# Optimization experiments

Measured on AMD Instinct MI355X. Metric: run time of the kernel, lower is better.

## Reference

```python
import jax, jax.numpy as jnp
import numpy as np
from functools import partial

A_CUBIC = -0.75  # PyTorch grid_sample bicubic coefficient

def _cubic_weights(t):
    # t in [0,1); returns 4 weights for taps at offsets -1,0,1,2
    a = A_CUBIC
    t2 = t * t; t3 = t2 * t
    w0 = a * (t3 - 2.0 * t2 + t)
    w1 = (a + 2.0) * t3 - (a + 3.0) * t2 + 1.0
    s = 1.0 - t
    w2 = (a + 2.0) * s * s * s - (a + 3.0) * s * s + 1.0
    u = 2.0 - t
    w3 = a * u * u * u - 5.0 * a * u * u + 8.0 * a * u - 4.0 * a
    return (w0, w1, w2, w3)

def grid_sample_bicubic(img, gx, gy):
    # img [N,C,H,W]; gx,gy [N,Ho,Wo] normalized coords in [-1,1]; border padding, align_corners=False
    N, C, H, W = img.shape
    ix = ((gx + 1.0) * W - 1.0) * 0.5
    iy = ((gy + 1.0) * H - 1.0) * 0.5
    x0 = jnp.floor(ix); tx = ix - x0
    y0 = jnp.floor(iy); ty = iy - y0
    x0i = x0.astype(jnp.int32); y0i = y0.astype(jnp.int32)
    wx = _cubic_weights(tx); wy = _cubic_weights(ty)
    gather = jax.vmap(lambda im, yi, xi: im[:, yi, xi])  # per-sample [C,Ho,Wo]
    out = jnp.zeros((N, C) + gx.shape[1:], img.dtype)
    for i in range(4):
        yi = jnp.clip(y0i + (i - 1), 0, H - 1)
        for j in range(4):
            xj = jnp.clip(x0i + (j - 1), 0, W - 1)
            v = gather(img, yi, xj)
            out = out + (wy[i] * wx[j])[:, None] * v
    return out

def jitter_aligned_interp(img, jitter, f):
    # F.affine_grid(identity+translation) + grid_sample bicubic, align_corners=False
    N, C, H, W = img.shape
    Ho, Wo = H * f, W * f
    bx = (2.0 * jnp.arange(Wo, dtype=img.dtype) + 1.0) / Wo - 1.0
    by = (2.0 * jnp.arange(Ho, dtype=img.dtype) + 1.0) / Ho - 1.0
    tx = 2.0 * (0.5 - jitter[:, 0]) / W
    ty = 2.0 * (0.5 - jitter[:, 1]) / H
    gx = jnp.broadcast_to(bx[None, None, :] + tx[:, None, None], (N, Ho, Wo))
    gy = jnp.broadcast_to(by[None, :, None] + ty[:, None, None], (N, Ho, Wo))
    return grid_sample_bicubic(img, gx, gy)

def zero_upsample(x, f):
    N, C, H, W = x.shape
    out = jnp.zeros((N, C, H * f, W * f), x.dtype)
    return out.at[:, :, ::f, ::f].set(x)

def jitter_align(img, jitter, f):
    # pad by f, per-sample crop at integer jitter offset (zero constant pad)
    N, C, H, W = img.shape
    ji = jnp.floor(jitter * f).astype(jnp.int32)  # [N,2] (x,y)
    padded = jnp.pad(img, ((0, 0), (0, 0), (f, f), (f, f)))
    def crop(im, j):
        sy = f - j[1]; sx = f - j[0]
        return jax.lax.dynamic_slice(im, (0, sy, sx), (C, H, W))
    return jax.vmap(crop)(padded, ji)

def resize_bilinear(x, f):
    # F.interpolate bilinear, align_corners=False (half-pixel, clamp to >=0 and edges)
    N, C, H, W = x.shape
    def coords(L):
        c = jnp.maximum((jnp.arange(L * f, dtype=x.dtype) + 0.5) / f - 0.5, 0.0)
        i0 = jnp.floor(c); t = c - i0
        i0 = i0.astype(jnp.int32)
        return jnp.clip(i0, 0, L - 1), jnp.clip(i0 + 1, 0, L - 1), t
    y0, y1, tyv = coords(H)
    x0, x1, txv = coords(W)
    xr = x[:, :, y0, :] * (1.0 - tyv)[None, None, :, None] + x[:, :, y1, :] * tyv[None, None, :, None]
    return xr[:, :, :, x0] * (1.0 - txv) + xr[:, :, :, x1] * txv

def conv3x3_reppad(x, w, b):
    x = jnp.pad(x, ((0, 0), (0, 0), (1, 1), (1, 1)), mode='edge')
    y = jax.lax.conv_general_dilated(x, w, (1, 1), 'VALID',
                                     dimension_numbers=('NCHW', 'OIHW', 'NCHW'))
    return y + b[None, :, None, None]

def sub_forward(frame, depth, mv, jitter, history, params, f):
    w1, b1, w2, b2, w3, b3 = params
    N = frame.shape[0]
    far, near = 100.0, 0.1
    d = near * far / (far - depth * (far - near))
    d = (d - near) / (far - near)
    frame4 = jnp.concatenate([frame, d], axis=1)  # [N,4,H,W]
    frame_bicubic = jitter_aligned_interp(frame4, jitter, f)  # [N,4,Hf,Wf]
    frame_up = jitter_align(zero_upsample(frame4, f), jitter, f)
    if history is None:
        history = frame_bicubic
    else:
        mv_hi = resize_bilinear(jnp.moveaxis(mv, 3, 1), f)       # [N,2,Hf,Wf]
        mv_hi = jnp.moveaxis(mv_hi, 1, 3)                        # [N,Hf,Wf,2]
        history = grid_sample_bicubic(history, mv_hi[..., 0], mv_hi[..., 1])
        oob = jnp.logical_or(mv_hi > 1.0, mv_hi < -1.0)
        mask = jnp.logical_or(oob[..., 0], oob[..., 1])[:, None]  # [N,1,Hf,Wf]
        history = jnp.where(mask, frame_bicubic, history)
    cnn_in = jnp.concatenate([frame_up, history], axis=1)  # [N,8,Hf,Wf]
    h = jax.nn.relu(conv3x3_reppad(cnn_in, w1, b1))
    h = jax.nn.relu(conv3x3_reppad(h, w2, b2))
    residual = conv3x3_reppad(h, w3, b3)  # [N,2,Hf,Wf]
    alpha = jnp.clip(residual[:, 0:1], 0.0, 1.0)
    history = history * (1.0 - alpha) + frame_bicubic * alpha
    history = jnp.concatenate([history[:, :3], history[:, 3:4] + residual[:, 1:2]], axis=1)
    history = jnp.clip(history, 0.0, 1.0)
    return history[:, :3], history

FACTOR = 2

def setup_inputs() -> dict:
    key = jax.random.key(0)
    ks = jax.random.split(key, 10)
    T, N, H, W = 3, 2, 360, 640
    frames = jax.random.uniform(ks[0], (T, N, 3, H, W), jnp.float32)
    depths = jax.random.uniform(ks[1], (T, N, 1, H, W), jnp.float32)
    mvs = jax.random.uniform(ks[2], (T, N, H, W, 2), jnp.float32, -1.05, 1.05)
    jitters = jax.random.uniform(ks[3], (T, N, 2), jnp.float32)
    w1 = jax.random.normal(ks[4], (64, 8, 3, 3), jnp.float32) * 0.1
    b1 = jnp.zeros((64,), jnp.float32)
    w2 = jax.random.normal(ks[5], (64, 64, 3, 3), jnp.float32) * 0.04
    b2 = jnp.zeros((64,), jnp.float32)
    w3 = jax.random.normal(ks[6], (2, 64, 3, 3), jnp.float32) * 0.04
    b3 = jnp.zeros((2,), jnp.float32)
    return {"frames": frames, "depths": depths, "mvs": mvs, "jitters": jitters,
            "w1": w1, "b1": b1, "w2": w2, "b2": b2, "w3": w3, "b3": b3}

def reference(frames, depths, mvs, jitters, w1, b1, w2, b2, w3, b3):
    params = (w1, b1, w2, b2, w3, b3)
    T = frames.shape[0]
    history = None
    outs = []
    for t in range(T - 1, -1, -1):  # torch forward iterates seq_length-1 .. 0
        recon, history = sub_forward(frames[t], depths[t], mvs[t], jitters[t], history, params, FACTOR)
        outs.append(recon)
    outs.reverse()
    return jnp.stack(outs)  # [T,N,3,H*f,W*f]
```

## Files before the change

kernel.cpp:

```cpp
#include <hip/hip_runtime.h>

#define T_STEPS 3
#define NB 2
#define H_LO 360
#define W_LO 640
#define H_HI 720
#define W_HI 1280
#define HW_LO (H_LO*W_LO)
#define HW_HI (H_HI*W_HI)
#define TILE 12

typedef _Float16 f16;
typedef __attribute__((ext_vector_type(4))) _Float16 f16x4;
typedef __attribute__((ext_vector_type(8))) _Float16 f16x8;
typedef __attribute__((ext_vector_type(4))) float f32x4;

#define OFF_H1  0
#define OFF_H2  0
#define OFF_CNN 32768
#define OFF_RES 32768
#define LDS_BYTES 37952

__device__ __forceinline__ int imin(int a,int b){return a<b?a:b;}
__device__ __forceinline__ int imax(int a,int b){return a>b?a:b;}
__device__ __forceinline__ int iclamp(int v,int lo,int hi){return imin(imax(v,lo),hi);}

__device__ __forceinline__ float depth_tx(float d0){
  float d = 10.0f / (100.0f - d0*99.9f);
  return (d - 0.1f) / 99.9f;
}

__device__ __forceinline__ void cubw(float t, float* w){
  const float a = -0.75f;
  float t2 = t*t, t3 = t2*t;
  w[0] = a*(t3 - 2.0f*t2 + t);
  w[1] = (a+2.0f)*t3 - (a+3.0f)*t2 + 1.0f;
  float s = 1.0f - t;
  w[2] = (a+2.0f)*s*s*s - (a+3.0f)*s*s + 1.0f;
  float u = 2.0f - t;
  w[3] = a*u*u*u - 5.0f*a*u*u + 8.0f*a*u - 4.0f*a;
}

__device__ __forceinline__ float4 fb_bicubic(const float* __restrict__ fbase,
    const float* __restrict__ dbase, float jx, float jy, int x, int y){
  float gx = (2.0f*(float)x + 1.0f)/(float)W_HI - 1.0f + 2.0f*(0.5f - jx)/(float)W_LO;
  float gy = (2.0f*(float)y + 1.0f)/(float)H_HI - 1.0f + 2.0f*(0.5f - jy)/(float)H_LO;
  float ix = ((gx + 1.0f)*(float)W_LO - 1.0f)*0.5f;
  float iy = ((gy + 1.0f)*(float)H_LO - 1.0f)*0.5f;
  float xf = floorf(ix), yf = floorf(iy);
  float tx = ix - xf, ty = iy - yf;
  int xi = (int)xf, yi = (int)yf;
  float wx[4], wy[4]; cubw(tx, wx); cubw(ty, wy);
  int xs[4], ys[4];
  #pragma unroll
  for (int j=0;j<4;j++){ xs[j]=iclamp(xi-1+j,0,W_LO-1); ys[j]=iclamp(yi-1+j,0,H_LO-1); }
  float a0=0.f,a1=0.f,a2=0.f,a3=0.f;
  #pragma unroll
  for (int i=0;i<4;i++){
    #pragma unroll
    for (int j=0;j<4;j++){
      float wgt = wy[i]*wx[j];
      int off = ys[i]*W_LO + xs[j];
      a0 += wgt*fbase[off];
      a1 += wgt*fbase[HW_LO+off];
      a2 += wgt*fbase[2*HW_LO+off];
      a3 += wgt*depth_tx(dbase[off]);
    }
  }
  return make_float4(a0,a1,a2,a3);
}

__global__ __launch_bounds__(256) void k_wprep(const float* __restrict__ w1g,
    const float* __restrict__ w2g, const float* __restrict__ w3g, f16* __restrict__ wbuf){
  int i = blockIdx.x*256 + threadIdx.x;
  if (i >= 46592) return;
  float val = 0.0f;
  if (i < 8192){
    int oc = i>>7, kk = i&127, k = kk ^ ((oc&7)<<3);
    if (k < 72) val = w1g[(oc*8 + (k&7))*9 + (k>>3)];
  } else if (i < 45056){
    int j = i - 8192; int oc = j/576, kk = j - oc*576, k = kk ^ ((oc&7)<<3);
    val = w2g[(oc*64 + (k&63))*9 + (k>>6)];
  } else {
    int j = i - 45056;
    if (j < 1152){ int nn = j/576, k = j - nn*576;
      val = w3g[(nn*64 + (k&63))*9 + (k>>6)];
    }
  }
  wbuf[i] = (f16)val;
}

__global__ __launch_bounds__(256) void k_pw(const float4* __restrict__ histA,
    const float* __restrict__ mv, const float* __restrict__ frame,
    const float* __restrict__ depth, const float* __restrict__ jit,
    float4* __restrict__ FB, float4* __restrict__ histB, int doWarp){
  int idx = blockIdx.x*256 + threadIdx.x;
  if (idx >= NB*HW_HI) return;
  int n = idx / HW_HI, p = idx - n*HW_HI;
  int y = p / W_HI, x = p - y*W_HI;
  const float* fbase = frame + (size_t)n*3*HW_LO;
  const float* dbase = depth + (size_t)n*HW_LO;
  float4 fb4 = fb_bicubic(fbase, dbase, jit[n*2], jit[n*2+1], x, y);
  FB[(size_t)n*HW_HI + p] = fb4;
  if (!doWarp) return;

  float cy = fmaxf(((float)y + 0.5f)/2.0f - 0.5f, 0.0f);
  float cx = fmaxf(((float)x + 0.5f)/2.0f - 0.5f, 0.0f);
  float y0f = floorf(cy), x0f = floorf(cx);
  float tyv = cy - y0f, txv = cx - x0f;
  int y0 = iclamp((int)y0f, 0, H_LO-1), y1 = iclamp((int)y0f+1, 0, H_LO-1);
  int x0 = iclamp((int)x0f, 0, W_LO-1), x1 = iclamp((int)x0f+1, 0, W_LO-1);
  const float* mb = mv + (size_t)n*HW_LO*2;
  float gx, gy;
  {
    float v00 = mb[(y0*W_LO+x0)*2], v01 = mb[(y0*W_LO+x1)*2];
    float v10 = mb[(y1*W_LO+x0)*2], v11 = mb[(y1*W_LO+x1)*2];
    float r0 = v00*(1.0f-tyv) + v10*tyv;
    float r1 = v01*(1.0f-tyv) + v11*tyv;
    gx = r0*(1.0f-txv) + r1*txv;
  }
  {
    float v00 = mb[(y0*W_LO+x0)*2+1], v01 = mb[(y0*W_LO+x1)*2+1];
    float v10 = mb[(y1*W_LO+x0)*2+1], v11 = mb[(y1*W_LO+x1)*2+1];
    float r0 = v00*(1.0f-tyv) + v10*tyv;
    float r1 = v01*(1.0f-tyv) + v11*tyv;
    gy = r0*(1.0f-txv) + r1*txv;
  }
  bool oob = (gx > 1.0f) || (gx < -1.0f) || (gy > 1.0f) || (gy < -1.0f);
  float4 res;
  if (oob) {
    res = fb4;
  } else {
    const float4* hb = histA + (size_t)n*HW_HI;
    float ix = ((gx + 1.0f)*(float)W_HI - 1.0f)*0.5f;
    float iy = ((gy + 1.0f)*(float)H_HI - 1.0f)*0.5f;
    float xf = floorf(ix), yf = floorf(iy);
    float tx = ix - xf, ty = iy - yf;
    int xi = (int)xf, yi = (int)yf;
    float wx[4], wy[4]; cubw(tx, wx); cubw(ty, wy);
    int xs[4], ys[4];
    #pragma unroll
    for (int j=0;j<4;j++){ xs[j]=iclamp(xi-1+j,0,W_HI-1); ys[j]=iclamp(yi-1+j,0,H_HI-1); }
    float a0=0.f,a1=0.f,a2=0.f,a3=0.f;
    #pragma unroll
    for (int i=0;i<4;i++){
      #pragma unroll
      for (int j=0;j<4;j++){
        float wgt = wy[i]*wx[j];
        float4 v = hb[ys[i]*W_HI + xs[j]];
        a0 += wgt*v.x; a1 += wgt*v.y; a2 += wgt*v.z; a3 += wgt*v.w;
      }
    }
    res = make_float4(a0,a1,a2,a3);
  }
  histB[(size_t)n*HW_HI + p] = res;
}

__global__ __launch_bounds__(256,3) void k_fused(
    const float* __restrict__ frame, const float* __restrict__ depth,
    const float* __restrict__ jit, const float4* __restrict__ histIn,
    const float4* __restrict__ FB, const f16* __restrict__ wbuf,
    const float* __restrict__ b1g, const float* __restrict__ b2g, const float* __restrict__ b3g,
    float4* __restrict__ histOut, float* __restrict__ outp)
{
  __shared__ __attribute__((aligned(16))) char smem[LDS_BYTES];
  const int tid = threadIdx.x;
  const int wv = tid>>6, ln = tid&63, lr = ln&15, lq = ln>>4;
  const int n  = blockIdx.z;
  const int r0 = blockIdx.y * TILE;
  const int c0 = blockIdx.x * TILE;
  const float jx = jit[n*2], jy = jit[n*2+1];
  const int jix = (int)floorf(jx*2.0f), jiy = (int)floorf(jy*2.0f);
  const float* fbase = frame + (size_t)n*3*HW_LO;
  const float* dbase = depth + (size_t)n*HW_LO;
  const float4* hist4 = histIn + (size_t)n*HW_HI;
  const int wkk = (lr&7)<<3;

  f16x8 B1[3][4];
  #pragma unroll
  for (int kc=0;kc<3;kc++)
    #pragma unroll
    for (int oct=0;oct<4;oct++){
      int oc = oct*16 + lr;
      int k0 = kc*32 + lq*8;
      B1[kc][oct] = *(const f16x8*)(wbuf + oc*128 + (k0 ^ wkk));
    }

  for (int e=tid; e<324; e+=256){
    int u = e/18, v = e - u*18;
    int cgy = iclamp(r0-3+u, 0, H_HI-1);
    int cgx = iclamp(c0-3+v, 0, W_HI-1);
    float v0=0.f, v1=0.f, v2=0.f, v3=0.f;
    int yy = cgy - jiy, xx = cgx - jix;
    if (yy>=0 && xx>=0 && !(yy&1) && !(xx&1)){
      int off = (yy>>1)*W_LO + (xx>>1);
      v0 = fbase[off]; v1 = fbase[HW_LO+off]; v2 = fbase[2*HW_LO+off];
      v3 = depth_tx(dbase[off]);
    }
    float4 h = hist4[cgy*W_HI + cgx];
    f16x8 pk;
    pk[0]=(f16)v0; pk[1]=(f16)v1; pk[2]=(f16)v2; pk[3]=(f16)v3;
    pk[4]=(f16)h.x; pk[5]=(f16)h.y; pk[6]=(f16)h.z; pk[7]=(f16)h.w;
    *(f16x8*)(smem + OFF_CNN + e*16) = pk;
  }
  __syncthreads();

  {
    float4 b1v[4];
    #pragma unroll
    for (int oct=0;oct<4;oct++) b1v[oct] = *(const float4*)(b1g + oct*16 + lq*4);
    #pragma unroll
    for (int ty4=0;ty4<4;ty4++){
      int ty = wv*4 + ty4;
      int g1y = iclamp(r0-2+ty, 0, H_HI-1);
      int g1x = iclamp(c0-2+lr, 0, W_HI-1);
      f32x4 acc[4];
      #pragma unroll
      for (int oct=0;oct<4;oct++) acc[oct] = (f32x4){b1v[oct].x,b1v[oct].y,b1v[oct].z,b1v[oct].w};
      #pragma unroll
      for (int kc=0;kc<3;kc++){
        int k0 = kc*32 + lq*8;
        int t = imin(k0>>3, 8);
        int dy = (t*11)>>5; int dx = t - dy*3;
        int uu = iclamp(g1y+dy-1, 0, H_HI-1) - (r0-3);
        int vv = iclamp(g1x+dx-1, 0, W_HI-1) - (c0-3);
        f16x8 a = *(const f16x8*)(smem + OFF_CNN + (uu*18+vv)*16);
        #pragma unroll
        for (int oct=0;oct<4;oct++)
          acc[oct] = __builtin_amdgcn_mfma_f32_16x16x32_f16(B1[kc][oct], a, acc[oct], 0,0,0);
      }
      #pragma unroll
      for (int oct=0;oct<4;oct++){
        f16x4 wv4;
        #pragma unroll
        for (int reg=0;reg<4;reg++) wv4[reg] = (f16)fmaxf(acc[oct][reg], 0.f);
        int oc0 = (oct*16 + lq*4) ^ ((lr&7)<<3);
        *(f16x4*)(smem + OFF_H1 + (((ty*16+lr)*64 + oc0)<<1)) = wv4;
      }
    }
  }
  __syncthreads();

  {
    const int nmt = (wv==0) ? 4 : 3;
    const int mtid[4] = {wv, 4+wv, 8+wv, 12};
    int rowOf[4][3], colc[4][3][2];
    #pragma unroll
    for (int mti=0;mti<4;mti++){
      int m = imin(mtid[mti]*16 + lr, 195);
      int py = m/14, px = m - py*14;
      int Ay = iclamp(r0-1+py, 0, H_HI-1);
      int Ax = iclamp(c0-1+px, 0, W_HI-1);
      #pragma unroll
      for (int d=0;d<3;d++){
        rowOf[mti][d] = (iclamp(Ay+d-1, 0, H_HI-1) - (r0-2))*1024;
        int vv = iclamp(Ax+d-1, 0, W_HI-1) - (c0-2);
        int key = (vv&7)<<3;
        colc[mti][d][0] = vv*64 + ((lq*8) ^ key);
        colc[mti][d][1] = vv*64 + ((32+lq*8) ^ key);
      }
    }
    float4 b2v[4];
    #pragma unroll
    for (int oct=0;oct<4;oct++) b2v[oct] = *(const float4*)(b2g + oct*16 + lq*4);
    f32x4 acc2[4][4];
    #pragma unroll
    for (int mti=0;mti<4;mti++)
      #pragma unroll
      for (int oct=0;oct<4;oct++) acc2[mti][oct] = (f32x4){b2v[oct].x,b2v[oct].y,b2v[oct].z,b2v[oct].w};
    const f16* w2b = wbuf + 8192;
    f16x8 bf[4];
    #pragma unroll
    for (int oct=0;oct<4;oct++)
      bf[oct] = *(const f16x8*)(w2b + (oct*16+lr)*576 + ((lq*8) ^ wkk));
    #pragma unroll
    for (int kc=0;kc<18;kc++){
      const int tap = kc>>1, half = kc&1;
      const int dy = tap/3, dx = tap - dy*3;
      f16x8 bfn[4];
      if (kc < 17){
        const int kn = kc+1, tapn = kn>>1, halfn = kn&1;
        #pragma unroll
        for (int oct=0;oct<4;oct++)
          bfn[oct] = *(const f16x8*)(w2b + (oct*16+lr)*576 + ((tapn*64 + halfn*32 + lq*8) ^ wkk));
      }
      #pragma unroll
      for (int mti=0;mti<4;mti++) if (mti < nmt){
        f16x8 a = *(const f16x8*)(smem + OFF_H1 + ((rowOf[mti][dy] + colc[mti][dx][half])<<1));
        #pragma unroll
        for (int oct=0;oct<4;oct++)
          acc2[mti][oct] = __builtin_amdgcn_mfma_f32_16x16x32_f16(bf[oct], a, acc2[mti][oct], 0,0,0);
      }
      #pragma unroll
      for (int oct=0;oct<4;oct++) bf[oct] = bfn[oct];
    }
    __syncthreads();
    #pragma unroll
    for (int mti=0;mti<4;mti++) if (mti < nmt){
      int m = mtid[mti]*16 + lr;
      if (m < 196){
        int py = m/14, px = m - py*14;
        int base = (py*14+px)*64; int key = (px&7)<<3;
        #pragma unroll
        for (int oct=0;oct<4;oct++){
          f16x4 wv4;
          #pragma unroll
          for (int reg=0;reg<4;reg++) wv4[reg] = (f16)fmaxf(acc2[mti][oct][reg], 0.f);
          *(f16x4*)(smem + OFF_H2 + ((base + ((oct*16 + lq*4) ^ key))<<1)) = wv4;
        }
      }
    }
  }
  __syncthreads();

  {
    const int nm3 = (wv==0) ? 3 : 2;
    const int m3t[3] = {wv, 4+wv, 8};
    int rowOf[3][3], colc[3][3][2];
    #pragma unroll
    for (int i=0;i<3;i++){
      int m = m3t[i]*16 + lr;
      int py = m/12, px = m - py*12;
      int Cy = r0 + py;
      int Cx = iclamp(c0+px, 0, W_HI-1);
      #pragma unroll
      for (int d=0;d<3;d++){
        rowOf[i][d] = (iclamp(Cy+d-1, 0, H_HI-1) - (r0-1))*896;
        int vv = iclamp(Cx+d-1, 0, W_HI-1) - (c0-1);
        int key = (vv&7)<<3;
        colc[i][d][0] = vv*64 + ((lq*8) ^ key);
        colc[i][d][1] = vv*64 + ((32+lq*8) ^ key);
      }
    }
    f32x4 acc3[3] = {{0,0,0,0},{0,0,0,0},{0,0,0,0}};
    const int cidx = ln&1;
    const f16* w3b = wbuf + 45056;
    f16x8 b = *(const f16x8*)(w3b + cidx*576 + lq*8);
    #pragma unroll
    for (int kc=0;kc<18;kc++){
      const int tap = kc>>1, half = kc&1;
      const int dy = tap/3, dx = tap - dy*3;
      f16x8 bn;
      if (kc < 17) bn = *(const f16x8*)(w3b + cidx*576 + (kc+1)*32 + lq*8);
      #pragma unroll
      for (int i=0;i<3;i++) if (i < nm3){
        f16x8 a = *(const f16x8*)(smem + OFF_H2 + ((rowOf[i][dy] + colc[i][dx][half])<<1));
        acc3[i] = __builtin_amdgcn_mfma_f32_16x16x32_f16(a, b, acc3[i], 0,0,0);
      }
      b = bn;
    }
    __syncthreads();
    float* sres = (float*)(smem + OFF_RES);
    if (lr < 2){
      float bv = b3g[lr];
      #pragma unroll
      for (int i=0;i<3;i++) if (i < nm3){
        #pragma unroll
        for (int reg=0;reg<4;reg++){
          int m = m3t[i]*16 + lq*4 + reg;
          sres[lr*144 + m] = acc3[i][reg] + bv;
        }
      }
    }
  }
  __syncthreads();

  if (tid < 144){
    int ty = tid/12, tx = tid - ty*12;
    int gy = r0 + ty, gx = c0 + tx;
    if (gx < W_HI){
      const float* sres = (const float*)(smem + OFF_RES);
      float a0 = sres[tid], a1 = sres[144+tid];
      float alpha = fminf(fmaxf(a0, 0.0f), 1.0f);
      int pix = gy*W_HI + gx;
      float4 fb = FB[(size_t)n*HW_HI + pix];
      float4 hv = hist4[pix];
      float h0 = hv.x*(1.0f-alpha) + fb.x*alpha;
      float h1 = hv.y*(1.0f-alpha) + fb.y*alpha;
      float h2 = hv.z*(1.0f-alpha) + fb.z*alpha;
      float h3 = hv.w*(1.0f-alpha) + fb.w*alpha + a1;
      h0 = fminf(fmaxf(h0,0.f),1.f); h1 = fminf(fmaxf(h1,0.f),1.f);
      h2 = fminf(fmaxf(h2,0.f),1.f); h3 = fminf(fmaxf(h3,0.f),1.f);
      histOut[(size_t)n*HW_HI + pix] = make_float4(h0,h1,h2,h3);
      float* rp = outp + (size_t)n*3*HW_HI + pix;
      rp[0] = h0; rp[HW_HI] = h1; rp[2*HW_HI] = h2;
    }
  }
}

extern "C" void kernel_launch(void* const* d_in, const int* in_sizes, int n_in,
                              void* d_out, int out_size, void* d_ws, size_t ws_size,
                              hipStream_t stream){
  const float* frames = (const float*)d_in[0];
  const float* depths = (const float*)d_in[1];
  const float* mvs    = (const float*)d_in[2];
  const float* jits   = (const float*)d_in[3];
  const float* w1 = (const float*)d_in[4];
  const float* b1 = (const float*)d_in[5];
  const float* w2 = (const float*)d_in[6];
  const float* b2 = (const float*)d_in[7];
  const float* w3 = (const float*)d_in[8];
  const float* b3 = (const float*)d_in[9];
  float* out = (float*)d_out;

  float4* FB4 = (float4*)d_ws;
  float4* HA  = FB4 + (size_t)NB*HW_HI;
  float4* HB  = HA  + (size_t)NB*HW_HI;
  f16*  wbuf = (f16*)(HB + (size_t)NB*HW_HI);

  dim3 bs(256);
  int npix = NB*HW_HI;
  dim3 gpix((npix + 255)/256);
  dim3 gfused((W_HI + TILE-1)/TILE, (H_HI + TILE-1)/TILE, NB);

  k_wprep<<<dim3((46592+255)/256), bs, 0, stream>>>(w1, w2, w3, wbuf);

  for (int t = T_STEPS-1; t >= 0; --t){
    const float* fr = frames + (size_t)t*NB*3*HW_LO;
    const float* dp = depths + (size_t)t*NB*HW_LO;
    const float* mv = mvs    + (size_t)t*NB*HW_LO*2;
    const float* jt = jits   + (size_t)t*NB*2;
    float* ot = out + (size_t)t*NB*3*HW_HI;
    int doWarp = (t != T_STEPS-1) ? 1 : 0;

    k_pw<<<gpix, bs, 0, stream>>>(HA, mv, fr, dp, jt, FB4, HB, doWarp);
    const float4* histIn = doWarp ? (const float4*)HB : (const float4*)FB4;
    k_fused<<<gfused, bs, 0, stream>>>(fr, dp, jt, histIn, FB4, wbuf,
        b1, b2, b3, HA, ot);
  }
}
```

Before: 1.273 ms.

## Enlarge output tile to 14x14 and remap MFMA row tiles across layers

```diff
diff --git a/kernel.cpp b/kernel.cpp
--- a/kernel.cpp
+++ b/kernel.cpp
@@ -8,7 +8,7 @@
 #define W_HI 1280
 #define HW_LO (H_LO*W_LO)
 #define HW_HI (H_HI*W_HI)
-#define TILE 12
+#define TILE 14
 
 typedef _Float16 f16;
 typedef __attribute__((ext_vector_type(4))) _Float16 f16x4;
@@ -17,9 +17,9 @@
 
 #define OFF_H1  0
 #define OFF_H2  0
-#define OFF_CNN 32768
-#define OFF_RES 32768
-#define LDS_BYTES 37952
+#define OFF_CNN 41472
+#define OFF_RES 41472
+#define LDS_BYTES 47872
 
 __device__ __forceinline__ int imin(int a,int b){return a<b?a:b;}
 __device__ __forceinline__ int imax(int a,int b){return a>b?a:b;}
@@ -186,8 +186,8 @@
       B1[kc][oct] = *(const f16x8*)(wbuf + oc*128 + (k0 ^ wkk));
     }
 
-  for (int e=tid; e<324; e+=256){
-    int u = e/18, v = e - u*18;
+  for (int e=tid; e<400; e+=256){
+    int u = e/20, v = e - u*20;
     int cgy = iclamp(r0-3+u, 0, H_HI-1);
     int cgx = iclamp(c0-3+v, 0, W_HI-1);
     float v0=0.f, v1=0.f, v2=0.f, v3=0.f;
@@ -209,11 +209,15 @@
     float4 b1v[4];
     #pragma unroll
     for (int oct=0;oct<4;oct++) b1v[oct] = *(const float4*)(b1g + oct*16 + lq*4);
-    #pragma unroll
-    for (int ty4=0;ty4<4;ty4++){
-      int ty = wv*4 + ty4;
-      int g1y = iclamp(r0-2+ty, 0, H_HI-1);
-      int g1x = iclamp(c0-2+lr, 0, W_HI-1);
+    const int nmt1 = (wv==0) ? 6 : 5;
+    #pragma unroll
+    for (int i=0;i<6;i++) if (i < nmt1){
+      int tile = (i<5) ? (4*i + wv) : 20;
+      int m = tile*16 + lr;
+      int mc = imin(m, 323);
+      int py = mc/18, px = mc - 18*py;
+      int Ay = iclamp(r0-2+py, 0, H_HI-1);
+      int Ax = iclamp(c0-2+px, 0, W_HI-1);
       f32x4 acc[4];
       #pragma unroll
       for (int oct=0;oct<4;oct++) acc[oct] = (f32x4){b1v[oct].x,b1v[oct].y,b1v[oct].z,b1v[oct].w};
@@ -222,38 +226,39 @@
         int k0 = kc*32 + lq*8;
         int t = imin(k0>>3, 8);
         int dy = (t*11)>>5; int dx = t - dy*3;
-        int uu = iclamp(g1y+dy-1, 0, H_HI-1) - (r0-3);
-        int vv = iclamp(g1x+dx-1, 0, W_HI-1) - (c0-3);
-        f16x8 a = *(const f16x8*)(smem + OFF_CNN + (uu*18+vv)*16);
+        int uu = iclamp(Ay+dy-1, 0, H_HI-1) - (r0-3);
+        int vv = iclamp(Ax+dx-1, 0, W_HI-1) - (c0-3);
+        f16x8 a = *(const f16x8*)(smem + OFF_CNN + (uu*20+vv)*16);
         #pragma unroll
         for (int oct=0;oct<4;oct++)
           acc[oct] = __builtin_amdgcn_mfma_f32_16x16x32_f16(B1[kc][oct], a, acc[oct], 0,0,0);
       }
-      #pragma unroll
-      for (int oct=0;oct<4;oct++){
-        f16x4 wv4;
-        #pragma unroll
-        for (int reg=0;reg<4;reg++) wv4[reg] = (f16)fmaxf(acc[oct][reg], 0.f);
-        int oc0 = (oct*16 + lq*4) ^ ((lr&7)<<3);
-        *(f16x4*)(smem + OFF_H1 + (((ty*16+lr)*64 + oc0)<<1)) = wv4;
+      if (m < 324){
+        #pragma unroll
+        for (int oct=0;oct<4;oct++){
+          f16x4 wv4;
+          #pragma unroll
+          for (int reg=0;reg<4;reg++) wv4[reg] = (f16)fmaxf(acc[oct][reg], 0.f);
+          int oc0 = (oct*16 + lq*4) ^ ((px&7)<<3);
+          *(f16x4*)(smem + OFF_H1 + ((m*64 + oc0)<<1)) = wv4;
+        }
       }
     }
   }
   __syncthreads();
 
   {
-    const int nmt = (wv==0) ? 4 : 3;
-    const int mtid[4] = {wv, 4+wv, 8+wv, 12};
+    const int mt0 = wv;
     int rowOf[4][3], colc[4][3][2];
     #pragma unroll
     for (int mti=0;mti<4;mti++){
-      int m = imin(mtid[mti]*16 + lr, 195);
-      int py = m/14, px = m - py*14;
+      int m = (mt0 + 4*mti)*16 + lr;
+      int py = m>>4, px = m&15;
       int Ay = iclamp(r0-1+py, 0, H_HI-1);
       int Ax = iclamp(c0-1+px, 0, W_HI-1);
       #pragma unroll
       for (int d=0;d<3;d++){
-        rowOf[mti][d] = (iclamp(Ay+d-1, 0, H_HI-1) - (r0-2))*1024;
+        rowOf[mti][d] = (iclamp(Ay+d-1, 0, H_HI-1) - (r0-2))*1152;
         int vv = iclamp(Ax+d-1, 0, W_HI-1) - (c0-2);
         int key = (vv&7)<<3;
         colc[mti][d][0] = vv*64 + ((lq*8) ^ key);
@@ -285,7 +290,7 @@
           bfn[oct] = *(const f16x8*)(w2b + (oct*16+lr)*576 + ((tapn*64 + halfn*32 + lq*8) ^ wkk));
       }
       #pragma unroll
-      for (int mti=0;mti<4;mti++) if (mti < nmt){
+      for (int mti=0;mti<4;mti++){
         f16x8 a = *(const f16x8*)(smem + OFF_H1 + ((rowOf[mti][dy] + colc[mti][dx][half])<<1));
         #pragma unroll
         for (int oct=0;oct<4;oct++)
@@ -296,43 +301,41 @@
     }
     __syncthreads();
     #pragma unroll
-    for (int mti=0;mti<4;mti++) if (mti < nmt){
-      int m = mtid[mti]*16 + lr;
-      if (m < 196){
-        int py = m/14, px = m - py*14;
-        int base = (py*14+px)*64; int key = (px&7)<<3;
-        #pragma unroll
-        for (int oct=0;oct<4;oct++){
-          f16x4 wv4;
-          #pragma unroll
-          for (int reg=0;reg<4;reg++) wv4[reg] = (f16)fmaxf(acc2[mti][oct][reg], 0.f);
-          *(f16x4*)(smem + OFF_H2 + ((base + ((oct*16 + lq*4) ^ key))<<1)) = wv4;
-        }
+    for (int mti=0;mti<4;mti++){
+      int m = (mt0 + 4*mti)*16 + lr;
+      int px = m&15;
+      int base = m*64; int key = (px&7)<<3;
+      #pragma unroll
+      for (int oct=0;oct<4;oct++){
+        f16x4 wv4;
+        #pragma unroll
+        for (int reg=0;reg<4;reg++) wv4[reg] = (f16)fmaxf(acc2[mti][oct][reg], 0.f);
+        *(f16x4*)(smem + OFF_H2 + ((base + ((oct*16 + lq*4) ^ key))<<1)) = wv4;
       }
     }
   }
   __syncthreads();
 
   {
-    const int nm3 = (wv==0) ? 3 : 2;
-    const int m3t[3] = {wv, 4+wv, 8};
-    int rowOf[3][3], colc[3][3][2];
-    #pragma unroll
-    for (int i=0;i<3;i++){
-      int m = m3t[i]*16 + lr;
-      int py = m/12, px = m - py*12;
-      int Cy = r0 + py;
+    const int nm3 = (wv==0) ? 4 : 3;
+    const int m3t[4] = {wv, 4+wv, 8+wv, 12};
+    int rowOf[4][3], colc[4][3][2];
+    #pragma unroll
+    for (int i=0;i<4;i++){
+      int m = imin(m3t[i]*16 + lr, 195);
+      int py = m/14, px = m - 14*py;
+      int Cy = iclamp(r0+py, 0, H_HI-1);
       int Cx = iclamp(c0+px, 0, W_HI-1);
       #pragma unroll
       for (int d=0;d<3;d++){
-        rowOf[i][d] = (iclamp(Cy+d-1, 0, H_HI-1) - (r0-1))*896;
+        rowOf[i][d] = (iclamp(Cy+d-1, 0, H_HI-1) - (r0-1))*1024;
         int vv = iclamp(Cx+d-1, 0, W_HI-1) - (c0-1);
         int key = (vv&7)<<3;
         colc[i][d][0] = vv*64 + ((lq*8) ^ key);
         colc[i][d][1] = vv*64 + ((32+lq*8) ^ key);
       }
     }
-    f32x4 acc3[3] = {{0,0,0,0},{0,0,0,0},{0,0,0,0}};
+    f32x4 acc3[4] = {{0,0,0,0},{0,0,0,0},{0,0,0,0},{0,0,0,0}};
     const int cidx = ln&1;
     const f16* w3b = wbuf + 45056;
     f16x8 b = *(const f16x8*)(w3b + cidx*576 + lq*8);
@@ -343,7 +346,7 @@
       f16x8 bn;
       if (kc < 17) bn = *(const f16x8*)(w3b + cidx*576 + (kc+1)*32 + lq*8);
       #pragma unroll
-      for (int i=0;i<3;i++) if (i < nm3){
+      for (int i=0;i<4;i++) if (i < nm3){
         f16x8 a = *(const f16x8*)(smem + OFF_H2 + ((rowOf[i][dy] + colc[i][dx][half])<<1));
         acc3[i] = __builtin_amdgcn_mfma_f32_16x16x32_f16(a, b, acc3[i], 0,0,0);
       }
@@ -354,23 +357,23 @@
     if (lr < 2){
       float bv = b3g[lr];
       #pragma unroll
-      for (int i=0;i<3;i++) if (i < nm3){
+      for (int i=0;i<4;i++) if (i < nm3){
         #pragma unroll
         for (int reg=0;reg<4;reg++){
           int m = m3t[i]*16 + lq*4 + reg;
-          sres[lr*144 + m] = acc3[i][reg] + bv;
+          if (m < 196) sres[lr*196 + m] = acc3[i][reg] + bv;
         }
       }
     }
   }
   __syncthreads();
 
-  if (tid < 144){
-    int ty = tid/12, tx = tid - ty*12;
+  if (tid < 196){
+    int ty = tid/14, tx = tid - 14*ty;
     int gy = r0 + ty, gx = c0 + tx;
-    if (gx < W_HI){
+    if (gy < H_HI && gx < W_HI){
       const float* sres = (const float*)(smem + OFF_RES);
-      float a0 = sres[tid], a1 = sres[144+tid];
+      float a0 = sres[tid], a1 = sres[196+tid];
       float alpha = fminf(fmaxf(a0, 0.0f), 1.0f);
       int pix = gy*W_HI + gx;
       float4 fb = FB[(size_t)n*HW_HI + pix];
```

Measured after the change: 1.126 ms. 1.13x faster.
